# Optimization experiments

Hardware: AMD Instinct MI355X
Metric: run time of the kernel (lower is better)

Reference implementation:

```python
import jax, jax.numpy as jnp
import numpy as np

B, C, H, W = 16, 512, 32, 32
NH, HD = 8, 64
CTX_DIM, L = 768, 512
EPS = 1e-5


def setup_inputs() -> dict:
    key = jax.random.key(0)
    ks = jax.random.split(key, 10)
    x = jax.random.normal(ks[0], (B, C, H, W), dtype=jnp.float32)
    context = jax.random.normal(ks[1], (B, L, CTX_DIM), dtype=jnp.float32)
    context_mask = jax.random.randint(ks[2], (B, L), 0, 2).astype(bool)
    context_mask = context_mask.at[:, 0].set(True)  # guarantee >=1 valid key per row
    s = 0.02
    ln_w = jnp.ones((C,), jnp.float32)
    ln_b = jnp.zeros((C,), jnp.float32)
    Wq = jax.random.normal(ks[3], (C, C), jnp.float32) * s
    Wk = jax.random.normal(ks[4], (C, C), jnp.float32) * s
    Wv = jax.random.normal(ks[5], (C, C), jnp.float32) * s
    Wo = jax.random.normal(ks[6], (C, C), jnp.float32) * s
    Wctx = jax.random.normal(ks[7], (C, CTX_DIM), jnp.float32) * s
    return {"x": x, "context": context, "context_mask": context_mask,
            "ln_w": ln_w, "ln_b": ln_b, "Wq": Wq, "Wk": Wk, "Wv": Wv,
            "Wo": Wo, "Wctx": Wctx}


def _layernorm(x, w, b):
    mu = jnp.mean(x, axis=-1, keepdims=True)
    var = jnp.mean(jnp.square(x - mu), axis=-1, keepdims=True)
    return (x - mu) * jax.lax.rsqrt(var + EPS) * w + b


def reference(x, context, context_mask, ln_w, ln_b, Wq, Wk, Wv, Wo, Wctx):
    b, c, h, w = x.shape
    n = h * w
    hidden = x.reshape(b, c, n).transpose(0, 2, 1)          # [b, n, c]
    hidden_norm = _layernorm(hidden, ln_w, ln_b)
    ctx = jnp.einsum('bld,cd->blc', context, Wctx)          # context_proj

    q = jnp.einsum('bnc,ec->bne', hidden_norm, Wq).reshape(b, n, NH, HD).transpose(0, 2, 1, 3)
    k = jnp.einsum('blc,ec->ble', ctx, Wk).reshape(b, -1, NH, HD).transpose(0, 2, 1, 3)
    v = jnp.einsum('blc,ec->ble', ctx, Wv).reshape(b, -1, NH, HD).transpose(0, 2, 1, 3)

    scale = HD ** -0.5
    scores = jnp.einsum('bhnd,bhld->bhnl', q, k) * scale    # [b,H,n,L]
    mask4 = context_mask[:, None, None, :]                  # [b,1,1,L]
    scores = jnp.where(mask4, scores, -jnp.inf)
    all_invalid = ~jnp.any(mask4, axis=-1, keepdims=True)   # [b,1,1,1]
    scores = jnp.where(all_invalid, 0.0, scores)
    attn = jax.nn.softmax(scores, axis=-1)
    attn = jnp.where(mask4, attn, 0.0)
    attn = jnp.where(all_invalid, 0.0, attn)

    out = jnp.einsum('bhnl,bhld->bhnd', attn, v)            # [b,H,n,hd]
    out = out.transpose(0, 2, 1, 3).reshape(b, n, c)
    out = jnp.einsum('bnc,ec->bne', out, Wo)
    out = out + hidden
    return out.transpose(0, 2, 1).reshape(b, c, h, w)
```

## Files before the change

kernel.cpp:

```cpp
#include <hip/hip_runtime.h>

#define B_   16
#define C_   512
#define N_   1024
#define L_   512
#define CTX_ 768
#define NH_  8
#define HD_  64
#define EPS_ 1e-5f

typedef short bfrag  __attribute__((ext_vector_type(8)));
typedef short bfrag4 __attribute__((ext_vector_type(4)));
typedef float f32x4  __attribute__((ext_vector_type(4)));

__device__ __forceinline__ ushort f2bf(float f) {
  union { float f; unsigned u; } v; v.f = f;
  unsigned r = v.u + 0x7fffu + ((v.u >> 16) & 1u);
  return (ushort)(r >> 16);
}

__device__ __forceinline__ f32x4 mfma16(bfrag a, bfrag b, f32x4 c) {
  return __builtin_amdgcn_mfma_f32_16x16x32_bf16(a, b, c, 0, 0, 0);
}
__device__ __forceinline__ f32x4 mfma16k16(bfrag4 a, bfrag4 b, f32x4 c) {
  return __builtin_amdgcn_mfma_f32_16x16x16bf16_1k(a, b, c, 0, 0, 0);
}
__device__ __forceinline__ unsigned cvt_pk_bf16(float lo, float hi) {
  unsigned d;
  asm("v_cvt_pk_bf16_f32 %0, %1, %2" : "=v"(d) : "v"(lo), "v"(hi));
  return d;
}

__device__ __forceinline__ void g2l16(const ushort* g, ushort* l) {
  __builtin_amdgcn_global_load_lds(
      (const __attribute__((address_space(1))) void*)g,
      (__attribute__((address_space(3))) void*)l, 16, 0, 0);
}

__global__ __launch_bounds__(256) void cast5_kernel(
    const float* __restrict__ s0, const float* __restrict__ s1,
    const float* __restrict__ s2, const float* __restrict__ s3,
    const float* __restrict__ s4,
    ushort* __restrict__ d0, ushort* __restrict__ d1, ushort* __restrict__ d2,
    ushort* __restrict__ d3, ushort* __restrict__ d4) {
  int i = blockIdx.x * 256 + threadIdx.x;
  const float* src; ushort* dst; int off;
  if      (i < 98304)  { src = s0; dst = d0; off = i; }
  else if (i < 163840) { src = s1; dst = d1; off = i - 98304; }
  else if (i < 229376) { src = s2; dst = d2; off = i - 163840; }
  else if (i < 294912) { src = s3; dst = d3; off = i - 229376; }
  else                 { src = s4; dst = d4; off = i - 294912; }
  float4 vv = ((const float4*)src)[off];
  ushort4 o;
  o.x = f2bf(vv.x); o.y = f2bf(vv.y); o.z = f2bf(vv.z); o.w = f2bf(vv.w);
  ((ushort4*)dst)[off] = o;
}

__global__ __launch_bounds__(1024) void ln_kernel(const float* __restrict__ x,
                                                  const float* __restrict__ w,
                                                  const float* __restrict__ bia,
                                                  ushort* __restrict__ hn) {
  const int b  = blockIdx.x;
  const int n0 = blockIdx.y * 64;
  const int tid = threadIdx.x;
  const int nx = tid & 63, cg = tid >> 6;
  const float* xb = x + (size_t)b * C_ * N_;

  float s = 0.f, s2 = 0.f;
  for (int c = cg; c < C_; c += 16) {
    float v = xb[(size_t)c * N_ + n0 + nx];
    s += v; s2 += v * v;
  }
  __shared__ float red[2][16][64];
  __shared__ float mean[64], rstd[64];
  red[0][cg][nx] = s; red[1][cg][nx] = s2;
  __syncthreads();
  if (cg == 0) {
    float ss = 0.f, ss2 = 0.f;
#pragma unroll
    for (int i = 0; i < 16; ++i) { ss += red[0][i][nx]; ss2 += red[1][i][nx]; }
    float mu  = ss * (1.f / C_);
    float var = ss2 * (1.f / C_) - mu * mu;
    mean[nx] = mu;
    rstd[nx] = rsqrtf(var + EPS_);
  }
  __syncthreads();

  __shared__ float tile[64][65];
  for (int ct = 0; ct < 8; ++ct) {
    const int c0 = ct * 64;
    for (int cy = cg; cy < 64; cy += 16)
      tile[cy][nx] = xb[(size_t)(c0 + cy) * N_ + n0 + nx];
    __syncthreads();
    const int cx = tid & 63, ng = tid >> 6;
    const float wv = w[c0 + cx], bv = bia[c0 + cx];
    for (int ny = ng; ny < 64; ny += 16) {
      float val = (tile[cx][ny] - mean[ny]) * rstd[ny] * wv + bv;
      hn[((size_t)b * N_ + n0 + ny) * C_ + c0 + cx] = f2bf(val);
    }
    __syncthreads();
  }
}

__device__ __forceinline__ void gemm_core(const ushort* __restrict__ A,
                                          const ushort* __restrict__ W,
                                          int K, ushort* la, ushort* lb,
                                          f32x4 acc[4][4],
                                          int tid, int wm, int we, int col, int rg) {
  const int lane = tid & 63, w = tid >> 6;
  const int rloc = lane >> 2, pt = lane & 3;
  const int pts = pt ^ ((rloc >> 1) & 3);
  const int qsel = (rg ^ ((col >> 1) & 3)) * 8;

  for (int k0 = 0; k0 < K; k0 += 32) {
#pragma unroll
    for (int c = 0; c < 2; ++c) {
      const int chunk = w + c * 4;
      const int row = chunk * 16 + rloc;
      g2l16(A + (size_t)row * K + k0 + pts * 8, la + chunk * 512);
      g2l16(W + (size_t)row * K + k0 + pts * 8, lb + chunk * 512);
    }
    __syncthreads();
    bfrag af[4], bf[4];
#pragma unroll
    for (int i = 0; i < 4; ++i) {
      af[i] = *(const bfrag*)&la[(wm + i * 16 + col) * 32 + qsel];
      bf[i] = *(const bfrag*)&lb[(we + i * 16 + col) * 32 + qsel];
    }
#pragma unroll
    for (int i = 0; i < 4; ++i)
#pragma unroll
      for (int j = 0; j < 4; ++j)
        acc[i][j] = mfma16(af[i], bf[j], acc[i][j]);
    __syncthreads();
  }
}

__global__ __launch_bounds__(256) void gemm_g(const ushort* __restrict__ A,
                                              const ushort* __restrict__ W,
                                              ushort* __restrict__ out, int K) {
  __shared__ ushort la[128 * 32];
  __shared__ ushort lb[128 * 32];
  const int m0 = blockIdx.x * 128, e0 = blockIdx.y * 128;
  const int tid = threadIdx.x, lane = tid & 63, w = tid >> 6;
  const int wm = (w >> 1) * 64, we = (w & 1) * 64;
  const int col = lane & 15, rg = lane >> 4;

  f32x4 acc[4][4] = {};
  gemm_core(A + (size_t)m0 * K, W + (size_t)e0 * K, K, la, lb, acc, tid, wm, we, col, rg);

#pragma unroll
  for (int i = 0; i < 4; ++i)
#pragma unroll
    for (int j = 0; j < 4; ++j)
#pragma unroll
      for (int r = 0; r < 4; ++r)
        out[(size_t)(m0 + wm + i * 16 + rg * 4 + r) * 512 + e0 + we + j * 16 + col] =
            f2bf(acc[i][j][r]);
}

__global__ __launch_bounds__(256) void gemm_kv(const ushort* __restrict__ A,
                                               const ushort* __restrict__ Wk,
                                               const ushort* __restrict__ Wv,
                                               ushort* __restrict__ Ko,
                                               ushort* __restrict__ Vo) {
  __shared__ ushort la[128 * 32];
  __shared__ ushort lb[128 * 32];
  const int isv = blockIdx.y >> 2;
  const ushort* W = isv ? Wv : Wk;
  ushort* out = isv ? Vo : Ko;
  const int m0 = blockIdx.x * 128, e0 = (blockIdx.y & 3) * 128;
  const int tid = threadIdx.x, lane = tid & 63, w = tid >> 6;
  const int wm = (w >> 1) * 64, we = (w & 1) * 64;
  const int col = lane & 15, rg = lane >> 4;

  f32x4 acc[4][4] = {};
  gemm_core(A + (size_t)m0 * C_, W + (size_t)e0 * C_, C_, la, lb, acc, tid, wm, we, col, rg);

#pragma unroll
  for (int i = 0; i < 4; ++i)
#pragma unroll
    for (int j = 0; j < 4; ++j)
#pragma unroll
      for (int r = 0; r < 4; ++r)
        out[(size_t)(m0 + wm + i * 16 + rg * 4 + r) * 512 + e0 + we + j * 16 + col] =
            f2bf(acc[i][j][r]);
}

__global__ __launch_bounds__(256) void gemm_res(const ushort* __restrict__ A,
                                                const ushort* __restrict__ W,
                                                const float* __restrict__ x,
                                                float* __restrict__ out) {
  __shared__ ushort la[128 * 32];
  __shared__ ushort lb[128 * 32];
  __shared__ float T[16][132];
  const int m0 = blockIdx.x * 128, e0 = blockIdx.y * 128;
  const int tid = threadIdx.x, lane = tid & 63, w = tid >> 6;
  const int wm = (w >> 1) * 64, we = (w & 1) * 64;
  const int col = lane & 15, rg = lane >> 4;

  f32x4 acc[4][4] = {};
  gemm_core(A + (size_t)m0 * C_, W + (size_t)e0 * C_, C_, la, lb, acc, tid, wm, we, col, rg);

  const int b = m0 >> 10, n0l = m0 & 1023;
#pragma unroll
  for (int g = 0; g < 8; ++g) {
    if ((w & 1) == (g >> 2)) {
      const int j = g & 3;
#pragma unroll
      for (int i = 0; i < 4; ++i)
        *(f32x4*)&T[col][wm + i * 16 + rg * 4] = acc[i][j];
    }
    __syncthreads();
    const int n = tid & 127;
    for (int cc = tid >> 7; cc < 16; cc += 2) {
      const int c = e0 + g * 16 + cc;
      const size_t idx = (size_t)b * C_ * N_ + (size_t)c * N_ + n0l + n;
      out[idx] = T[cc][n] + x[idx];
    }
    __syncthreads();
  }
}

__global__ __launch_bounds__(256) void gemm_ctx(const float* __restrict__ Ap,
                                                const ushort* __restrict__ W,
                                                ushort* __restrict__ outp) {
  __shared__ ushort la[128 * 40];
  __shared__ ushort lb[128 * 40];
  const int m0 = blockIdx.x * 128, e0 = blockIdx.y * 128;
  const int tid = threadIdx.x, lane = tid & 63, w = tid >> 6;
  const int wm = (w >> 1) * 64, we = (w & 1) * 64;
  const int col = lane & 15, rg = lane >> 4;
  const int srow = tid >> 1, sh = (tid & 1) * 16;
  const int K = CTX_;

  f32x4 acc[4][4] = {};

  for (int k0 = 0; k0 < K; k0 += 32) {
    {
      const float* ap = &Ap[(size_t)(m0 + srow) * K + k0 + sh];
      float4 f0 = ((const float4*)ap)[0];
      float4 f1 = ((const float4*)ap)[1];
      float4 f2 = ((const float4*)ap)[2];
      float4 f3 = ((const float4*)ap)[3];
      union { int4 v; ushort u[8]; } p0, p1;
      p0.u[0] = f2bf(f0.x); p0.u[1] = f2bf(f0.y); p0.u[2] = f2bf(f0.z); p0.u[3] = f2bf(f0.w);
      p0.u[4] = f2bf(f1.x); p0.u[5] = f2bf(f1.y); p0.u[6] = f2bf(f1.z); p0.u[7] = f2bf(f1.w);
      p1.u[0] = f2bf(f2.x); p1.u[1] = f2bf(f2.y); p1.u[2] = f2bf(f2.z); p1.u[3] = f2bf(f2.w);
      p1.u[4] = f2bf(f3.x); p1.u[5] = f2bf(f3.y); p1.u[6] = f2bf(f3.z); p1.u[7] = f2bf(f3.w);
      *(int4*)&la[srow * 40 + sh]     = p0.v;
      *(int4*)&la[srow * 40 + sh + 8] = p1.v;
      const ushort* wp = &W[(size_t)(e0 + srow) * K + k0 + sh];
      *(int4*)&lb[srow * 40 + sh]     = *(const int4*)wp;
      *(int4*)&lb[srow * 40 + sh + 8] = *(const int4*)(wp + 8);
    }
    __syncthreads();
    bfrag af[4], bf[4];
#pragma unroll
    for (int i = 0; i < 4; ++i) {
      af[i] = *(const bfrag*)&la[(wm + i * 16 + col) * 40 + rg * 8];
      bf[i] = *(const bfrag*)&lb[(we + i * 16 + col) * 40 + rg * 8];
    }
#pragma unroll
    for (int i = 0; i < 4; ++i)
#pragma unroll
      for (int j = 0; j < 4; ++j)
        acc[i][j] = mfma16(af[i], bf[j], acc[i][j]);
    __syncthreads();
  }

#pragma unroll
  for (int i = 0; i < 4; ++i)
#pragma unroll
    for (int j = 0; j < 4; ++j)
#pragma unroll
      for (int r = 0; r < 4; ++r)
        outp[(size_t)(m0 + wm + i * 16 + rg * 4 + r) * 512 + e0 + we + j * 16 + col] =
            f2bf(acc[i][j][r]);
}

__global__ __launch_bounds__(256) void attn_mfma(const ushort* __restrict__ q,
                                                 const ushort* __restrict__ k,
                                                 const ushort* __restrict__ v,
                                                 const int* __restrict__ mask,
                                                 ushort* __restrict__ o) {
  __shared__ ushort Kl[64 * 72];
  __shared__ ushort Vt[64 * 72];
  __shared__ float mlb[64];

  const int h = blockIdx.y, b = blockIdx.z;
  const int q0 = blockIdx.x * 128;
  const int tid = threadIdx.x, lane = tid & 63, w = tid >> 6;
  const int col = lane & 15, rg = lane >> 4;
  const int wq = w * 32;
  const float C1 = 0.18033688011112042f;

  bfrag qf[2][2];
#pragma unroll
  for (int mi = 0; mi < 2; ++mi)
#pragma unroll
    for (int kc = 0; kc < 2; ++kc)
      qf[mi][kc] = *(const bfrag*)
          &q[((size_t)b * N_ + q0 + wq + mi * 16 + col) * C_ + h * HD_ + kc * 32 + rg * 8];

  f32x4 oa[2][4] = {};
  float l_part[2] = {0.f, 0.f};

  for (int l0 = 0; l0 < L_; l0 += 64) {
#pragma unroll
    for (int it = 0; it < 2; ++it) {
      const int idx = it * 256 + tid;
      const int key = idx >> 3, part = idx & 7;
      *(int4*)&Kl[key * 72 + part * 8] =
          *(const int4*)&k[((size_t)b * L_ + l0 + key) * C_ + h * HD_ + part * 8];
    }
#pragma unroll
    for (int it = 0; it < 4; ++it) {
      const int idx = it * 256 + tid;
      const int key = idx & 63, d0 = (idx >> 6) * 4;
      ushort4 vv = *(const ushort4*)&v[((size_t)b * L_ + l0 + key) * C_ + h * HD_ + d0];
      Vt[(d0 + 0) * 72 + key] = vv.x;
      Vt[(d0 + 1) * 72 + key] = vv.y;
      Vt[(d0 + 2) * 72 + key] = vv.z;
      Vt[(d0 + 3) * 72 + key] = vv.w;
    }
    if (tid < 64) mlb[tid] = mask[b * L_ + l0 + tid] ? 0.f : -1e30f;
    __syncthreads();

    f32x4 s2[2][4] = {};
#pragma unroll
    for (int kc = 0; kc < 2; ++kc) {
      bfrag kf[4];
#pragma unroll
      for (int ni = 0; ni < 4; ++ni)
        kf[ni] = *(const bfrag*)&Kl[(ni * 16 + col) * 72 + kc * 32 + rg * 8];
#pragma unroll
      for (int mi = 0; mi < 2; ++mi)
#pragma unroll
        for (int ni = 0; ni < 4; ++ni)
          s2[mi][ni] = mfma16(kf[ni], qf[mi][kc], s2[mi][ni]);
    }
    bfrag4 pf[2][4];
#pragma unroll
    for (int ni = 0; ni < 4; ++ni) {
      const f32x4 bias4 = *(const f32x4*)&mlb[ni * 16 + rg * 4];
#pragma unroll
      for (int mi = 0; mi < 2; ++mi) {
        const float p0 = exp2f(fmaf(s2[mi][ni][0], C1, bias4[0]));
        const float p1 = exp2f(fmaf(s2[mi][ni][1], C1, bias4[1]));
        const float p2 = exp2f(fmaf(s2[mi][ni][2], C1, bias4[2]));
        const float p3 = exp2f(fmaf(s2[mi][ni][3], C1, bias4[3]));
        l_part[mi] += (p0 + p1) + (p2 + p3);
        union { bfrag4 v; unsigned u[2]; } pk;
        pk.u[0] = cvt_pk_bf16(p0, p1);
        pk.u[1] = cvt_pk_bf16(p2, p3);
        pf[mi][ni] = pk.v;
      }
    }
#pragma unroll
    for (int ni = 0; ni < 4; ++ni) {
      bfrag4 vf[4];
#pragma unroll
      for (int di = 0; di < 4; ++di)
        vf[di] = *(const bfrag4*)&Vt[(di * 16 + col) * 72 + ni * 16 + rg * 4];
#pragma unroll
      for (int mi = 0; mi < 2; ++mi)
#pragma unroll
        for (int di = 0; di < 4; ++di)
          oa[mi][di] = mfma16k16(pf[mi][ni], vf[di], oa[mi][di]);
    }
    __syncthreads();
  }

  float linv[2][4];
#pragma unroll
  for (int mi = 0; mi < 2; ++mi) {
    float l = l_part[mi];
    l += __shfl_xor(l, 16);
    l += __shfl_xor(l, 32);
#pragma unroll
    for (int r = 0; r < 4; ++r) {
      int lv = __builtin_amdgcn_ds_bpermute((rg * 4 + r) * 4, __float_as_int(l));
      linv[mi][r] = 1.f / __int_as_float(lv);
    }
  }
#pragma unroll
  for (int mi = 0; mi < 2; ++mi)
#pragma unroll
    for (int r = 0; r < 4; ++r) {
      const size_t row = (size_t)b * N_ + q0 + wq + mi * 16 + rg * 4 + r;
#pragma unroll
      for (int di = 0; di < 4; ++di)
        o[row * C_ + h * HD_ + di * 16 + col] = f2bf(oa[mi][di][r] * linv[mi][r]);
    }
}

extern "C" void kernel_launch(void* const* d_in, const int* in_sizes, int n_in,
                              void* d_out, int out_size, void* d_ws, size_t ws_size,
                              hipStream_t stream) {
  (void)in_sizes; (void)n_in; (void)out_size; (void)ws_size;
  const float* x       = (const float*)d_in[0];
  const float* context = (const float*)d_in[1];
  const int*   mask    = (const int*)d_in[2];
  const float* ln_w    = (const float*)d_in[3];
  const float* ln_b    = (const float*)d_in[4];
  const float* Wq      = (const float*)d_in[5];
  const float* Wk      = (const float*)d_in[6];
  const float* Wv      = (const float*)d_in[7];
  const float* Wo      = (const float*)d_in[8];
  const float* Wctx    = (const float*)d_in[9];

  char* wsb = (char*)d_ws;
  ushort* qb    = (ushort*)(wsb + 0);
  ushort* kb    = (ushort*)(wsb + 16777216);
  ushort* vb    = (ushort*)(wsb + 25165824);
  ushort* hn    = (ushort*)(wsb + 33554432);
  ushort* ctx   = (ushort*)(wsb + 50331648);
  ushort* wctxb = (ushort*)(wsb + 58720256);
  ushort* wqb   = (ushort*)(wsb + 59506688);
  ushort* wkb   = (ushort*)(wsb + 60030976);
  ushort* wvb   = (ushort*)(wsb + 60555264);
  ushort* wob   = (ushort*)(wsb + 61079552);

  cast5_kernel<<<1408, 256, 0, stream>>>(Wctx, Wq, Wk, Wv, Wo,
                                         wctxb, wqb, wkb, wvb, wob);
  ln_kernel<<<dim3(B_, N_ / 64), 1024, 0, stream>>>(x, ln_w, ln_b, hn);
  gemm_ctx<<<dim3(64, 4), 256, 0, stream>>>(context, wctxb, ctx);
  gemm_kv<<<dim3(64, 8), 256, 0, stream>>>(ctx, wkb, wvb, kb, vb);
  gemm_g<<<dim3(128, 4), 256, 0, stream>>>(hn, wqb, qb, C_);
  attn_mfma<<<dim3(N_ / 128, NH_, B_), 256, 0, stream>>>(qb, kb, vb, mask, hn);
  gemm_res<<<dim3(128, 4), 256, 0, stream>>>(hn, wob, x, (float*)d_out);
}
```

Before: 174.4 us.

## Fuse LayerNorm apply into Q projection GEMM, keep only stats kernel

The LayerNorm kernel now only computes per-token mean and rstd. Normalisation, the affine transform and the bf16 cast move into the A-tile load of a new Q-projection GEMM that reads fp32 x directly. This removes writing and rereading the normalised hidden tensor in bf16. In exchange, each of the 4 column-blocks re-reads x in fp32 (twice the bytes of bf16, four times over) with scalar strided loads and no async g2l path, which could slow the GEMM main loop.

```diff
diff --git a/kernel.cpp b/kernel.cpp
--- a/kernel.cpp
+++ b/kernel.cpp
@@ -56,10 +56,9 @@
   ((ushort4*)dst)[off] = o;
 }
 
-__global__ __launch_bounds__(1024) void ln_kernel(const float* __restrict__ x,
-                                                  const float* __restrict__ w,
-                                                  const float* __restrict__ bia,
-                                                  ushort* __restrict__ hn) {
+__global__ __launch_bounds__(1024) void ln_stats(const float* __restrict__ x,
+                                                 float* __restrict__ mu_out,
+                                                 float* __restrict__ rs_out) {
   const int b  = blockIdx.x;
   const int n0 = blockIdx.y * 64;
   const int tid = threadIdx.x;
@@ -72,33 +71,16 @@
     s += v; s2 += v * v;
   }
   __shared__ float red[2][16][64];
-  __shared__ float mean[64], rstd[64];
   red[0][cg][nx] = s; red[1][cg][nx] = s2;
   __syncthreads();
   if (cg == 0) {
     float ss = 0.f, ss2 = 0.f;
 #pragma unroll
     for (int i = 0; i < 16; ++i) { ss += red[0][i][nx]; ss2 += red[1][i][nx]; }
-    float mu  = ss * (1.f / C_);
-    float var = ss2 * (1.f / C_) - mu * mu;
-    mean[nx] = mu;
-    rstd[nx] = rsqrtf(var + EPS_);
-  }
-  __syncthreads();
-
-  __shared__ float tile[64][65];
-  for (int ct = 0; ct < 8; ++ct) {
-    const int c0 = ct * 64;
-    for (int cy = cg; cy < 64; cy += 16)
-      tile[cy][nx] = xb[(size_t)(c0 + cy) * N_ + n0 + nx];
-    __syncthreads();
-    const int cx = tid & 63, ng = tid >> 6;
-    const float wv = w[c0 + cx], bv = bia[c0 + cx];
-    for (int ny = ng; ny < 64; ny += 16) {
-      float val = (tile[cx][ny] - mean[ny]) * rstd[ny] * wv + bv;
-      hn[((size_t)b * N_ + n0 + ny) * C_ + c0 + cx] = f2bf(val);
-    }
-    __syncthreads();
+    float m  = ss * (1.f / C_);
+    float var = ss2 * (1.f / C_) - m * m;
+    mu_out[(size_t)b * N_ + n0 + nx] = m;
+    rs_out[(size_t)b * N_ + n0 + nx] = rsqrtf(var + EPS_);
   }
 }
 
@@ -134,29 +116,6 @@
         acc[i][j] = mfma16(af[i], bf[j], acc[i][j]);
     __syncthreads();
   }
-}
-
-__global__ __launch_bounds__(256) void gemm_g(const ushort* __restrict__ A,
-                                              const ushort* __restrict__ W,
-                                              ushort* __restrict__ out, int K) {
-  __shared__ ushort la[128 * 32];
-  __shared__ ushort lb[128 * 32];
-  const int m0 = blockIdx.x * 128, e0 = blockIdx.y * 128;
-  const int tid = threadIdx.x, lane = tid & 63, w = tid >> 6;
-  const int wm = (w >> 1) * 64, we = (w & 1) * 64;
-  const int col = lane & 15, rg = lane >> 4;
-
-  f32x4 acc[4][4] = {};
-  gemm_core(A + (size_t)m0 * K, W + (size_t)e0 * K, K, la, lb, acc, tid, wm, we, col, rg);
-
-#pragma unroll
-  for (int i = 0; i < 4; ++i)
-#pragma unroll
-    for (int j = 0; j < 4; ++j)
-#pragma unroll
-      for (int r = 0; r < 4; ++r)
-        out[(size_t)(m0 + wm + i * 16 + rg * 4 + r) * 512 + e0 + we + j * 16 + col] =
-            f2bf(acc[i][j][r]);
 }
 
 __global__ __launch_bounds__(256) void gemm_kv(const ushort* __restrict__ A,
@@ -279,6 +238,71 @@
             f2bf(acc[i][j][r]);
 }
 
+__global__ __launch_bounds__(256) void gemm_lnq(const float* __restrict__ x,
+                                                const float* __restrict__ mu,
+                                                const float* __restrict__ rs,
+                                                const float* __restrict__ lnw,
+                                                const float* __restrict__ lnb,
+                                                const ushort* __restrict__ W,
+                                                ushort* __restrict__ out) {
+  __shared__ ushort la[128 * 40];
+  __shared__ ushort lb[128 * 40];
+  const int m0 = blockIdx.x * 128, e0 = blockIdx.y * 128;
+  const int b = m0 >> 10, n0l = m0 & 1023;
+  const int tid = threadIdx.x, lane = tid & 63, w = tid >> 6;
+  const int wm = (w >> 1) * 64, we = (w & 1) * 64;
+  const int col = lane & 15, rg = lane >> 4;
+  const int nloc = tid & 127, chalf = (tid >> 7) * 16;
+  const int srow = tid >> 1, sh = (tid & 1) * 16;
+
+  const float muv = mu[(size_t)b * N_ + n0l + nloc];
+  const float rsv = rs[(size_t)b * N_ + n0l + nloc];
+  const float nmr = -muv * rsv;
+  const float* xb = x + (size_t)b * C_ * N_ + n0l + nloc;
+
+  f32x4 acc[4][4] = {};
+
+  for (int k0 = 0; k0 < C_; k0 += 32) {
+    {
+      union { int4 v[2]; ushort u[16]; } pk;
+#pragma unroll
+      for (int i = 0; i < 16; ++i) {
+        const int c = k0 + chalf + i;
+        const float xv = xb[(size_t)c * N_];
+        const float t = fmaf(xv, rsv, nmr);
+        pk.u[i] = f2bf(fmaf(t, lnw[c], lnb[c]));
+      }
+      *(int4*)&la[nloc * 40 + chalf]     = pk.v[0];
+      *(int4*)&la[nloc * 40 + chalf + 8] = pk.v[1];
+      const ushort* wp = &W[(size_t)(e0 + srow) * C_ + k0 + sh];
+      *(int4*)&lb[srow * 40 + sh]     = *(const int4*)wp;
+      *(int4*)&lb[srow * 40 + sh + 8] = *(const int4*)(wp + 8);
+    }
+    __syncthreads();
+    bfrag af[4], bf[4];
+#pragma unroll
+    for (int i = 0; i < 4; ++i) {
+      af[i] = *(const bfrag*)&la[(wm + i * 16 + col) * 40 + rg * 8];
+      bf[i] = *(const bfrag*)&lb[(we + i * 16 + col) * 40 + rg * 8];
+    }
+#pragma unroll
+    for (int i = 0; i < 4; ++i)
+#pragma unroll
+      for (int j = 0; j < 4; ++j)
+        acc[i][j] = mfma16(af[i], bf[j], acc[i][j]);
+    __syncthreads();
+  }
+
+#pragma unroll
+  for (int i = 0; i < 4; ++i)
+#pragma unroll
+    for (int j = 0; j < 4; ++j)
+#pragma unroll
+      for (int r = 0; r < 4; ++r)
+        out[(size_t)(m0 + wm + i * 16 + rg * 4 + r) * 512 + e0 + we + j * 16 + col] =
+            f2bf(acc[i][j][r]);
+}
+
 __global__ __launch_bounds__(256) void attn_mfma(const ushort* __restrict__ q,
                                                  const ushort* __restrict__ k,
                                                  const ushort* __restrict__ v,
@@ -414,20 +438,22 @@
   ushort* qb    = (ushort*)(wsb + 0);
   ushort* kb    = (ushort*)(wsb + 16777216);
   ushort* vb    = (ushort*)(wsb + 25165824);
-  ushort* hn    = (ushort*)(wsb + 33554432);
+  ushort* atto  = (ushort*)(wsb + 33554432);
   ushort* ctx   = (ushort*)(wsb + 50331648);
   ushort* wctxb = (ushort*)(wsb + 58720256);
   ushort* wqb   = (ushort*)(wsb + 59506688);
   ushort* wkb   = (ushort*)(wsb + 60030976);
   ushort* wvb   = (ushort*)(wsb + 60555264);
   ushort* wob   = (ushort*)(wsb + 61079552);
+  float*  mub   = (float*)(wsb + 61603840);
+  float*  rsb   = (float*)(wsb + 61669376);
 
   cast5_kernel<<<1408, 256, 0, stream>>>(Wctx, Wq, Wk, Wv, Wo,
                                          wctxb, wqb, wkb, wvb, wob);
-  ln_kernel<<<dim3(B_, N_ / 64), 1024, 0, stream>>>(x, ln_w, ln_b, hn);
+  ln_stats<<<dim3(B_, N_ / 64), 1024, 0, stream>>>(x, mub, rsb);
   gemm_ctx<<<dim3(64, 4), 256, 0, stream>>>(context, wctxb, ctx);
   gemm_kv<<<dim3(64, 8), 256, 0, stream>>>(ctx, wkb, wvb, kb, vb);
-  gemm_g<<<dim3(128, 4), 256, 0, stream>>>(hn, wqb, qb, C_);
-  attn_mfma<<<dim3(N_ / 128, NH_, B_), 256, 0, stream>>>(qb, kb, vb, mask, hn);
-  gemm_res<<<dim3(128, 4), 256, 0, stream>>>(hn, wob, x, (float*)d_out);
-}
+  gemm_lnq<<<dim3(128, 4), 256, 0, stream>>>(x, mub, rsb, ln_w, ln_b, wqb, qb);
+  attn_mfma<<<dim3(N_ / 128, NH_, B_), 256, 0, stream>>>(qb, kb, vb, mask, atto);
+  gemm_res<<<dim3(128, 4), 256, 0, stream>>>(atto, wob, x, (float*)d_out);
+}
```

Result: faster. 170.8 us (-2.1%).
